# Performance work log

Measured on AMD Instinct MI355X. Metric: run time of the kernel, lower is better.

## Reference

```python
import jax, jax.numpy as jnp
import numpy as np

DIM = 768
HEADS = 12
HIDDEN = 4 * DIM
B, D, H, W = 4, 8, 14, 14


def setup_inputs() -> dict:
    key = jax.random.key(0)
    ks = jax.random.split(key, 16)
    s = lambda k, shape, fan: jax.random.normal(k, shape, jnp.float32) * (1.0 / np.sqrt(fan))
    return {
        "x": jax.random.normal(ks[0], (B, DIM, D, H, W), jnp.float32),
        "pos_w": s(ks[1], (DIM, 1, 3, 3, 3), 27),   # depthwise conv3d weight (OIDHW, groups=DIM)
        "pos_b": jnp.zeros((DIM,), jnp.float32),
        "ln1_w": jnp.ones((DIM,), jnp.float32),
        "ln1_b": jnp.zeros((DIM,), jnp.float32),
        "qkv_w": s(ks[2], (3 * DIM, DIM), DIM),      # torch Linear layout [out,in], no bias
        "proj_w": s(ks[3], (DIM, DIM), DIM),
        "proj_b": jnp.zeros((DIM,), jnp.float32),
        "ln2_w": jnp.ones((DIM,), jnp.float32),
        "ln2_b": jnp.zeros((DIM,), jnp.float32),
        "fc1_w": s(ks[4], (HIDDEN, DIM), DIM),
        "fc1_b": jnp.zeros((HIDDEN,), jnp.float32),
        "fc2_w": s(ks[5], (DIM, HIDDEN), HIDDEN),
        "fc2_b": jnp.zeros((DIM,), jnp.float32),
    }


def _layernorm(x, w, b, eps=1e-5):
    mu = jnp.mean(x, axis=-1, keepdims=True)
    var = jnp.var(x, axis=-1, keepdims=True)
    return (x - mu) * jax.lax.rsqrt(var + eps) * w + b


def _forward(x, pos_w, pos_b, ln1_w, ln1_b, qkv_w, proj_w, proj_b,
             ln2_w, ln2_b, fc1_w, fc1_b, fc2_w, fc2_b):
    Bs, C, Ds, Hs, Ws = x.shape
    # depthwise 3x3x3 conv positional embedding + residual
    pe = jax.lax.conv_general_dilated(
        x, pos_w, window_strides=(1, 1, 1), padding=[(1, 1)] * 3,
        dimension_numbers=("NCDHW", "OIDHW", "NCDHW"), feature_group_count=C)
    x = x + pe + pos_b[None, :, None, None, None] * 0 + jnp.zeros((), x.dtype)
    x = x + 0.0  # keep simple
    x = x - pe + pe + pos_b[None, :, None, None, None]  # fold bias into conv output
    # flatten to tokens [B, N, C]
    t = x.reshape(Bs, C, -1).transpose(0, 2, 1)
    N = t.shape[1]
    # attention
    h = _layernorm(t, ln1_w, ln1_b)
    qkv = (h @ qkv_w.T).reshape(Bs, N, 3, HEADS, C // HEADS)
    q, k, v = [qkv[:, :, i].transpose(0, 2, 1, 3) for i in range(3)]  # [B,h,N,d]
    scale = (C // HEADS) ** -0.5
    attn = jax.nn.softmax(jnp.einsum("bhnd,bhmd->bhnm", q, k) * scale, axis=-1)
    o = jnp.einsum("bhnm,bhmd->bhnd", attn, v).transpose(0, 2, 1, 3).reshape(Bs, N, C)
    t = t + o @ proj_w.T + proj_b
    # MLP
    h = _layernorm(t, ln2_w, ln2_b)
    h = jax.nn.gelu(h @ fc1_w.T + fc1_b, approximate=False)
    t = t + h @ fc2_w.T + fc2_b
    return t.transpose(0, 2, 1).reshape(Bs, C, Ds, Hs, Ws)


def reference(x, pos_w, pos_b, ln1_w, ln1_b, qkv_w, proj_w, proj_b,
              ln2_w, ln2_b, fc1_w, fc1_b, fc2_w, fc2_b):
    return _forward(x, pos_w, pos_b, ln1_w, ln1_b, qkv_w, proj_w, proj_b,
                    ln2_w, ln2_b, fc1_w, fc1_b, fc2_w, fc2_b)
```

## Files before the change

### kernel.cpp

```cpp
#include <hip/hip_runtime.h>
#include <hip/hip_bf16.h>


using bf16 = __hip_bfloat16;
typedef __bf16 bf16x8 __attribute__((ext_vector_type(8)));
typedef float f32x4 __attribute__((ext_vector_type(4)));

#define NTOK 1568
#define CDIM 768
#define NH 12
#define HD 64
#define HID 3072
#define BN 6272

static __device__ __forceinline__ float bf2f(bf16 x) { return __bfloat162float(x); }
static __device__ __forceinline__ bf16 f2bf(float x) { return __float2bfloat16(x); }
static __device__ __forceinline__ unsigned short bfbits(float f) {
  bf16 h = __float2bfloat16(f);
  return *reinterpret_cast<unsigned short*>(&h);
}
static __device__ __forceinline__ float u16f(unsigned short u) {
  return __uint_as_float(((unsigned)u) << 16);
}
static __device__ __forceinline__ bool probe_bf16(const unsigned* p) {
  return ((*p) & 0xFFFFu) == 0x3F80u;
}

struct IngestArgs {
  const void* src[13];
  bf16* dst[13];
  int off[14];
};
__global__ __launch_bounds__(256) void ingest_all(IngestArgs a, const unsigned* __restrict__ probe) {
  bool isbf = probe_bf16(probe);
  int i = blockIdx.x * 256 + threadIdx.x;
  if (i >= a.off[13]) return;
  int j = 0;
  #pragma unroll
  for (int s = 0; s < 12; s++) if (i >= a.off[s + 1]) j = s + 1;
  int li = i - a.off[j];
  if (isbf) a.dst[j][li] = ((const bf16*)a.src[j])[li];
  else      a.dst[j][li] = f2bf(((const float*)a.src[j])[li]);
}

#define CXS 597
__global__ __launch_bounds__(256) void conv_pe_kernel(
    const void* __restrict__ x, const bf16* __restrict__ pw,
    const bf16* __restrict__ pb, float* __restrict__ t,
    const unsigned* __restrict__ probe) {
  int c0 = blockIdx.x * 16;
  int bd = blockIdx.y;
  int b = bd >> 3, d = bd & 7;
  bool isbf = probe_bf16(probe);
  __shared__ float xs[16 * CXS];
  int tid = threadIdx.x;

  for (int idx = tid; idx < 2352; idx += 256) {
    int ci = idx / 147;
    int rem = idx - ci * 147;
    int dd = rem / 49;
    int f4 = rem - dd * 49;
    int ds = d - 1 + dd;
    float4 v = make_float4(0.f, 0.f, 0.f, 0.f);
    if ((unsigned)ds < 8u) {
      size_t off = ((size_t)(b * CDIM + c0 + ci) * 8 + ds) * 196 + f4 * 4;
      if (isbf) {
        const bf16* xp = (const bf16*)x + off;
        v = make_float4(bf2f(xp[0]), bf2f(xp[1]), bf2f(xp[2]), bf2f(xp[3]));
      } else {
        v = *reinterpret_cast<const float4*>((const float*)x + off);
      }
    }
    float* dst = &xs[ci * CXS + dd * 196 + f4 * 4];
    dst[0] = v.x; dst[1] = v.y; dst[2] = v.z; dst[3] = v.w;
  }

  int ci = tid & 15;
  float wl[27];
  #pragma unroll
  for (int j = 0; j < 27; j++) wl[j] = bf2f(pw[(c0 + ci) * 27 + j]);
  float pbci = bf2f(pb[c0 + ci]);
  __syncthreads();

  const float* xc = &xs[ci * CXS];
  for (int n = (tid >> 4); n < 196; n += 16) {
    int hh = n / 14, ww = n - hh * 14;
    float acc = xc[196 + n] + pbci;
    #pragma unroll
    for (int kh = -1; kh <= 1; kh++) {
      int h2 = hh + kh;
      if ((unsigned)h2 >= 14u) continue;
      #pragma unroll
      for (int kw = -1; kw <= 1; kw++) {
        int w2 = ww + kw;
        if ((unsigned)w2 >= 14u) continue;
        int base = h2 * 14 + w2;
        int wj = (kh + 1) * 3 + (kw + 1);
        acc += wl[wj]      * xc[base];
        acc += wl[9 + wj]  * xc[196 + base];
        acc += wl[18 + wj] * xc[392 + base];
      }
    }
    t[((size_t)b * NTOK + d * 196 + n) * CDIM + c0 + ci] = acc;
  }
}

__global__ __launch_bounds__(256) void ln_kernel(
    const float* __restrict__ t, const bf16* __restrict__ w,
    const bf16* __restrict__ bia, bf16* __restrict__ h) {
  int tid = threadIdx.x, wid = tid >> 6, lane = tid & 63;
  int m = blockIdx.x * 4 + wid;
  const float4* row4 = reinterpret_cast<const float4*>(t + (size_t)m * CDIM);
  float4 v0 = row4[lane], v1 = row4[lane + 64], v2 = row4[lane + 128];
  float s = v0.x + v0.y + v0.z + v0.w + v1.x + v1.y + v1.z + v1.w + v2.x + v2.y + v2.z + v2.w;
  float q = v0.x*v0.x + v0.y*v0.y + v0.z*v0.z + v0.w*v0.w +
            v1.x*v1.x + v1.y*v1.y + v1.z*v1.z + v1.w*v1.w +
            v2.x*v2.x + v2.y*v2.y + v2.z*v2.z + v2.w*v2.w;
  #pragma unroll
  for (int off = 32; off > 0; off >>= 1) {
    s += __shfl_xor(s, off);
    q += __shfl_xor(q, off);
  }
  float mu = s * (1.f / CDIM);
  float var = q * (1.f / CDIM) - mu * mu;
  float rstd = rsqrtf(fmaxf(var, 0.f) + 1e-5f);
  const ushort4* w4 = reinterpret_cast<const ushort4*>(w);
  const ushort4* b4 = reinterpret_cast<const ushort4*>(bia);
  ushort4* h4 = reinterpret_cast<ushort4*>(h + (size_t)m * CDIM);
  #pragma unroll
  for (int j = 0; j < 3; j++) {
    float4 v = (j == 0) ? v0 : (j == 1) ? v1 : v2;
    ushort4 ww = w4[lane + 64 * j];
    ushort4 bb = b4[lane + 64 * j];
    ushort4 oo;
    oo.x = bfbits((v.x - mu) * rstd * u16f(ww.x) + u16f(bb.x));
    oo.y = bfbits((v.y - mu) * rstd * u16f(ww.y) + u16f(bb.y));
    oo.z = bfbits((v.z - mu) * rstd * u16f(ww.z) + u16f(bb.z));
    oo.w = bfbits((v.w - mu) * rstd * u16f(ww.w) + u16f(bb.w));
    h4[lane + 64 * j] = oo;
  }
}

#define LDA 40

template <int EPI>
__global__ __launch_bounds__(256) void gemm128(
    const bf16* __restrict__ A, const bf16* __restrict__ W,
    const bf16* __restrict__ bias, float* __restrict__ resid,
    bf16* __restrict__ oq, bf16* __restrict__ okk, bf16* __restrict__ ovt,
    bf16* __restrict__ obf, int K) {
  __shared__ __align__(16) bf16 As[128 * LDA];
  __shared__ __align__(16) bf16 Bs[128 * LDA];
  int tid = threadIdx.x;
  int w = tid >> 6, lane = tid & 63, quad = lane >> 4, l16 = lane & 15;
  int wr = w >> 1, wc = w & 1;
  int m0 = blockIdx.x * 128, n0 = blockIdx.y * 128;

  int r0 = tid >> 2;
  int c0 = (tid & 3) * 8;
  const bf16* gA0 = A + (size_t)(m0 + r0) * K + c0;
  const bf16* gA1 = A + (size_t)(m0 + 64 + r0) * K + c0;
  const bf16* gB0 = W + (size_t)(n0 + r0) * K + c0;
  const bf16* gB1 = W + (size_t)(n0 + 64 + r0) * K + c0;
  bf16* lA0 = As + r0 * LDA + c0;
  bf16* lA1 = As + (64 + r0) * LDA + c0;
  bf16* lB0 = Bs + r0 * LDA + c0;
  bf16* lB1 = Bs + (64 + r0) * LDA + c0;

  f32x4 acc[4][4];
  #pragma unroll
  for (int mi = 0; mi < 4; mi++)
    #pragma unroll
    for (int ni = 0; ni < 4; ni++) acc[mi][ni] = (f32x4){0.f, 0.f, 0.f, 0.f};

  bf16x8 ra0 = *reinterpret_cast<const bf16x8*>(gA0);
  bf16x8 ra1 = *reinterpret_cast<const bf16x8*>(gA1);
  bf16x8 rb0 = *reinterpret_cast<const bf16x8*>(gB0);
  bf16x8 rb1 = *reinterpret_cast<const bf16x8*>(gB1);

  for (int k0 = 0; k0 < K; k0 += 32) {
    *reinterpret_cast<bf16x8*>(lA0) = ra0;
    *reinterpret_cast<bf16x8*>(lA1) = ra1;
    *reinterpret_cast<bf16x8*>(lB0) = rb0;
    *reinterpret_cast<bf16x8*>(lB1) = rb1;
    __syncthreads();
    if (k0 + 32 < K) {
      ra0 = *reinterpret_cast<const bf16x8*>(gA0 + k0 + 32);
      ra1 = *reinterpret_cast<const bf16x8*>(gA1 + k0 + 32);
      rb0 = *reinterpret_cast<const bf16x8*>(gB0 + k0 + 32);
      rb1 = *reinterpret_cast<const bf16x8*>(gB1 + k0 + 32);
    }
    bf16x8 af[4], bfr[4];
    #pragma unroll
    for (int mi = 0; mi < 4; mi++)
      af[mi] = *reinterpret_cast<const bf16x8*>(As + (wr * 64 + mi * 16 + l16) * LDA + quad * 8);
    #pragma unroll
    for (int ni = 0; ni < 4; ni++)
      bfr[ni] = *reinterpret_cast<const bf16x8*>(Bs + (wc * 64 + ni * 16 + l16) * LDA + quad * 8);
    #pragma unroll
    for (int mi = 0; mi < 4; mi++)
      #pragma unroll
      for (int ni = 0; ni < 4; ni++)
        acc[mi][ni] = __builtin_amdgcn_mfma_f32_16x16x32_bf16(af[mi], bfr[ni], acc[mi][ni], 0, 0, 0);
    __syncthreads();
  }

  int mrow0 = m0 + wr * 64 + quad * 4;
  #pragma unroll
  for (int mi = 0; mi < 4; mi++) {
    #pragma unroll
    for (int ni = 0; ni < 4; ni++) {
      int col0 = n0 + wc * 64 + ni * 16;
      int col = col0 + l16;
      if (EPI == 0) {
        int i3 = col0 / CDIM;
        int rem = col0 % CDIM;
        int head = rem >> 6;
        int ddb = rem & 63;
        if (i3 == 2) {
          int m4 = mrow0 + mi * 16;
          int b = m4 / NTOK, n4 = m4 % NTOK;
          ushort4 pk;
          pk.x = bfbits(acc[mi][ni][0]);
          pk.y = bfbits(acc[mi][ni][1]);
          pk.z = bfbits(acc[mi][ni][2]);
          pk.w = bfbits(acc[mi][ni][3]);
          size_t idx = ((size_t)(b * NH + head) * HD + ddb + l16) * NTOK + n4;
          *reinterpret_cast<ushort4*>(ovt + idx) = pk;
        } else {
          bf16* dst = (i3 == 0) ? oq : okk;
          float scale = (i3 == 0) ? 0.125f : 1.0f;
          int dd = ddb + l16;
          #pragma unroll
          for (int reg = 0; reg < 4; reg++) {
            int m = mrow0 + mi * 16 + reg;
            int b = m / NTOK, n = m % NTOK;
            dst[((size_t)(b * NH + head) * NTOK + n) * HD + dd] = f2bf(acc[mi][ni][reg] * scale);
          }
        }
      } else if (EPI == 1) {
        float bb = bf2f(bias[col]);
        #pragma unroll
        for (int reg = 0; reg < 4; reg++) {
          int m = mrow0 + mi * 16 + reg;
          size_t idx = (size_t)m * CDIM + col;
          resid[idx] = resid[idx] + acc[mi][ni][reg] + bb;
        }
      } else if (EPI == 2) {
        float bb = bf2f(bias[col]);
        #pragma unroll
        for (int reg = 0; reg < 4; reg++) {
          int m = mrow0 + mi * 16 + reg;
          float xg = acc[mi][ni][reg] + bb;
          float ge = 0.5f * xg * (1.0f + erff(xg * 0.70710678118f));
          obf[(size_t)m * HID + col] = f2bf(ge);
        }
      } else {
        float bb = bf2f(bias[col]);
        #pragma unroll
        for (int reg = 0; reg < 4; reg++) {
          int m = mrow0 + mi * 16 + reg;
          size_t idx = (size_t)m * CDIM + col;
          obf[idx] = f2bf(resid[idx] + acc[mi][ni][reg] + bb);
        }
      }
    }
  }
}

#define LDS_S 80
__global__ __launch_bounds__(256) void attn_mfma(
    const bf16* __restrict__ q, const bf16* __restrict__ k,
    const bf16* __restrict__ vt, bf16* __restrict__ o) {
  __shared__ __align__(16) bf16 Ks[64 * LDS_S];
  __shared__ __align__(16) bf16 Vs[64 * LDS_S];
  __shared__ __align__(16) bf16 Ps[4][16 * LDS_S];
  int tid = threadIdx.x;
  int w = tid >> 6, lane = tid & 63, quad = lane >> 4, l16 = lane & 15;
  int qt = blockIdx.x;
  int bh = blockIdx.y;
  int b = bh / NH, head = bh % NH;
  const size_t kbase = (size_t)bh * NTOK * HD;

  int qr = qt * 64 + w * 16 + l16;
  int qrc = min(qr, NTOK - 1);
  bf16x8 aq0 = *reinterpret_cast<const bf16x8*>(q + kbase + (size_t)qrc * HD + quad * 8);
  bf16x8 aq1 = *reinterpret_cast<const bf16x8*>(q + kbase + (size_t)qrc * HD + 32 + quad * 8);

  f32x4 oacc[4];
  #pragma unroll
  for (int di = 0; di < 4; di++) oacc[di] = (f32x4){0.f, 0.f, 0.f, 0.f};
  float lrow[4] = {0.f, 0.f, 0.f, 0.f};

  int sr0 = tid >> 3;
  int sc0 = (tid & 7) * 8;
  const bf16* gK = k + kbase + (size_t)sr0 * HD + sc0;
  const bf16* gV = vt + ((size_t)bh * HD + sr0) * NTOK + sc0;
  bf16* pw = Ps[w];

  for (int t = 0; t < 25; t++) {
    int m0 = t * 64;
    __syncthreads();
    *reinterpret_cast<bf16x8*>(Ks + sr0 * LDS_S + sc0) =
        *reinterpret_cast<const bf16x8*>(gK + (size_t)m0 * HD);
    *reinterpret_cast<bf16x8*>(Ks + (sr0 + 32) * LDS_S + sc0) =
        *reinterpret_cast<const bf16x8*>(gK + (size_t)(m0 + 32) * HD);
    *reinterpret_cast<bf16x8*>(Vs + sr0 * LDS_S + sc0) =
        *reinterpret_cast<const bf16x8*>(gV + m0);
    *reinterpret_cast<bf16x8*>(Vs + (sr0 + 32) * LDS_S + sc0) =
        *reinterpret_cast<const bf16x8*>(gV + 32 * (size_t)NTOK + m0);
    __syncthreads();

    f32x4 s[4];
    #pragma unroll
    for (int ni = 0; ni < 4; ni++) {
      bf16x8 b0 = *reinterpret_cast<const bf16x8*>(Ks + (ni * 16 + l16) * LDS_S + quad * 8);
      bf16x8 b1 = *reinterpret_cast<const bf16x8*>(Ks + (ni * 16 + l16) * LDS_S + 32 + quad * 8);
      f32x4 z = (f32x4){0.f, 0.f, 0.f, 0.f};
      z = __builtin_amdgcn_mfma_f32_16x16x32_bf16(aq0, b0, z, 0, 0, 0);
      z = __builtin_amdgcn_mfma_f32_16x16x32_bf16(aq1, b1, z, 0, 0, 0);
      s[ni] = z;
    }
    if (t == 24) {
      s[2] = (f32x4){-1e30f, -1e30f, -1e30f, -1e30f};
      s[3] = (f32x4){-1e30f, -1e30f, -1e30f, -1e30f};
    }

    #pragma unroll
    for (int ni = 0; ni < 4; ni++)
      #pragma unroll
      for (int r = 0; r < 4; r++)
        s[ni][r] = __expf(s[ni][r] - 12.0f);
    #pragma unroll
    for (int r = 0; r < 4; r++)
      lrow[r] += s[0][r] + s[1][r] + s[2][r] + s[3][r];

    #pragma unroll
    for (int ni = 0; ni < 4; ni++)
      #pragma unroll
      for (int r = 0; r < 4; r++)
        pw[(quad * 4 + r) * LDS_S + ni * 16 + l16] = f2bf(s[ni][r]);
    bf16x8 ap0 = *reinterpret_cast<const bf16x8*>(pw + l16 * LDS_S + quad * 8);
    bf16x8 ap1 = *reinterpret_cast<const bf16x8*>(pw + l16 * LDS_S + 32 + quad * 8);

    #pragma unroll
    for (int di = 0; di < 4; di++) {
      bf16x8 bv0 = *reinterpret_cast<const bf16x8*>(Vs + (di * 16 + l16) * LDS_S + quad * 8);
      bf16x8 bv1 = *reinterpret_cast<const bf16x8*>(Vs + (di * 16 + l16) * LDS_S + 32 + quad * 8);
      oacc[di] = __builtin_amdgcn_mfma_f32_16x16x32_bf16(ap0, bv0, oacc[di], 0, 0, 0);
      oacc[di] = __builtin_amdgcn_mfma_f32_16x16x32_bf16(ap1, bv1, oacc[di], 0, 0, 0);
    }
  }

  #pragma unroll
  for (int r = 0; r < 4; r++) {
    float t_ = lrow[r];
    t_ += __shfl_xor(t_, 1);
    t_ += __shfl_xor(t_, 2);
    t_ += __shfl_xor(t_, 4);
    t_ += __shfl_xor(t_, 8);
    lrow[r] = t_;
  }

  int orow0 = qt * 64 + w * 16 + quad * 4;
  #pragma unroll
  for (int r = 0; r < 4; r++) {
    int row = orow0 + r;
    if (row < NTOK) {
      float inv = 1.0f / lrow[r];
      size_t obase = ((size_t)b * NTOK + row) * CDIM + head * HD + l16;
      #pragma unroll
      for (int di = 0; di < 4; di++)
        o[obase + di * 16] = f2bf(oacc[di][r] * inv);
    }
  }
}

__global__ __launch_bounds__(256) void out_transpose(
    const bf16* __restrict__ t3, bf16* __restrict__ ob, float* __restrict__ of,
    const unsigned* __restrict__ probe) {
  bool isbf = probe_bf16(probe);
  __shared__ float tile[32][33];
  int c0 = blockIdx.x * 32;
  int n0 = blockIdx.y * 32;
  int b = blockIdx.z;
  int tx = threadIdx.x & 31;
  int ty = threadIdx.x >> 5;
  for (int yy = ty; yy < 32; yy += 8)
    tile[yy][tx] = bf2f(t3[((size_t)b * NTOK + n0 + yy) * CDIM + c0 + tx]);
  __syncthreads();
  for (int yy = ty; yy < 32; yy += 8) {
    size_t oi = ((size_t)b * CDIM + c0 + yy) * NTOK + n0 + tx;
    float vv = tile[tx][yy];
    if (isbf) ob[oi] = f2bf(vv);
    else      of[oi] = vv;
  }
}

extern "C" void kernel_launch(void* const* d_in, const int* in_sizes, int n_in,
                              void* d_out, int out_size, void* d_ws, size_t ws_size,
                              hipStream_t stream) {
  const unsigned* probe = (const unsigned*)d_in[3];

  char* ws = (char*)d_ws;
  size_t cur = 0;
  auto alloc = [&](size_t bytes) -> char* {
    char* p = ws + cur;
    cur = (cur + bytes + 511) & ~(size_t)511;
    return p;
  };

  bf16* canon[14];
  IngestArgs ia;
  int tot = 0;
  canon[0] = nullptr;
  for (int i = 1; i < 14; i++) {
    canon[i] = (bf16*)alloc((size_t)in_sizes[i] * 2);
    ia.src[i - 1] = d_in[i];
    ia.dst[i - 1] = canon[i];
    ia.off[i - 1] = tot;
    tot += in_sizes[i];
  }
  ia.off[13] = tot;

  float* t  = (float*)alloc((size_t)BN * CDIM * 4);
  bf16*  R1 = (bf16*)alloc((size_t)BN * CDIM * 2);
  bf16*  R2 = (bf16*)alloc((size_t)BN * HID * 2);
  bf16* q  = R2;
  bf16* kk = R2 + (size_t)BN * CDIM;
  bf16* vt = R2 + (size_t)2 * BN * CDIM;
  bf16* g  = R2;
  (void)ws_size;

  ingest_all<<<(tot + 255) / 256, 256, 0, stream>>>(ia, probe);
  const bf16 *pos_w = canon[1], *pos_b = canon[2],
             *ln1_w = canon[3], *ln1_b = canon[4], *qkv_w = canon[5],
             *proj_w = canon[6], *proj_b = canon[7], *ln2_w = canon[8],
             *ln2_b = canon[9], *fc1_w = canon[10], *fc1_b = canon[11],
             *fc2_w = canon[12], *fc2_b = canon[13];

  conv_pe_kernel<<<dim3(CDIM / 16, 32), 256, 0, stream>>>(d_in[0], pos_w, pos_b, t, probe);
  ln_kernel<<<BN / 4, 256, 0, stream>>>(t, ln1_w, ln1_b, R1);
  gemm128<0><<<dim3(BN / 128, 2304 / 128), 256, 0, stream>>>(
      R1, qkv_w, nullptr, nullptr, q, kk, vt, nullptr, CDIM);
  attn_mfma<<<dim3(25, 4 * NH), 256, 0, stream>>>(q, kk, vt, R1);
  gemm128<1><<<dim3(BN / 128, CDIM / 128), 256, 0, stream>>>(
      R1, proj_w, proj_b, t, nullptr, nullptr, nullptr, nullptr, CDIM);
  ln_kernel<<<BN / 4, 256, 0, stream>>>(t, ln2_w, ln2_b, R1);
  gemm128<2><<<dim3(BN / 128, HID / 128), 256, 0, stream>>>(
      R1, fc1_w, fc1_b, nullptr, nullptr, nullptr, nullptr, g, CDIM);
  gemm128<3><<<dim3(BN / 128, CDIM / 128), 256, 0, stream>>>(
      g, fc2_w, fc2_b, t, nullptr, nullptr, nullptr, R1, HID);
  out_transpose<<<dim3(CDIM / 32, NTOK / 32, 4), 256, 0, stream>>>(
      R1, (bf16*)d_out, (float*)d_out, probe);
}
```

Before: 436.4 us.

## Stage GEMM tiles with direct global-to-LDS loads and double buffering

The tiled bf16 GEMM no longer loads tiles through registers. It now uses 16-byte global_load_lds into two LDS buffers, so the next K-slice is fetched while MFMAs run on the current one, with one barrier per iteration. The LDS tiles lose their row padding so each wave's contiguous 16-byte-per-lane writes line up. This is meant to remove register staging and expose more memory/compute overlap. It risks LDS bank conflicts on the unpadded fragment reads, and correctness depends on the loads having completed at the barrier.

```diff
diff --git a/kernel.cpp b/kernel.cpp
--- a/kernel.cpp
+++ b/kernel.cpp
@@ -24,6 +24,12 @@
 }
 static __device__ __forceinline__ bool probe_bf16(const unsigned* p) {
   return ((*p) & 0xFFFFu) == 0x3F80u;
+}
+
+typedef const __attribute__((address_space(1))) void* gas1_t;
+typedef __attribute__((address_space(3))) void* las3_t;
+static __device__ __forceinline__ void gload_lds16(const bf16* g, bf16* l) {
+  __builtin_amdgcn_global_load_lds((gas1_t)(const void*)g, (las3_t)(void*)l, 16, 0, 0);
 }
 
 struct IngestArgs {
@@ -141,7 +147,7 @@
   }
 }
 
-#define LDA 40
+#define BK 32
 
 template <int EPI>
 __global__ __launch_bounds__(256) void gemm128(
@@ -149,23 +155,21 @@
     const bf16* __restrict__ bias, float* __restrict__ resid,
     bf16* __restrict__ oq, bf16* __restrict__ okk, bf16* __restrict__ ovt,
     bf16* __restrict__ obf, int K) {
-  __shared__ __align__(16) bf16 As[128 * LDA];
-  __shared__ __align__(16) bf16 Bs[128 * LDA];
+  __shared__ __align__(16) bf16 As[2][128 * BK];
+  __shared__ __align__(16) bf16 Bs[2][128 * BK];
   int tid = threadIdx.x;
   int w = tid >> 6, lane = tid & 63, quad = lane >> 4, l16 = lane & 15;
   int wr = w >> 1, wc = w & 1;
   int m0 = blockIdx.x * 128, n0 = blockIdx.y * 128;
 
-  int r0 = tid >> 2;
-  int c0 = (tid & 3) * 8;
-  const bf16* gA0 = A + (size_t)(m0 + r0) * K + c0;
-  const bf16* gA1 = A + (size_t)(m0 + 64 + r0) * K + c0;
-  const bf16* gB0 = W + (size_t)(n0 + r0) * K + c0;
-  const bf16* gB1 = W + (size_t)(n0 + 64 + r0) * K + c0;
-  bf16* lA0 = As + r0 * LDA + c0;
-  bf16* lA1 = As + (64 + r0) * LDA + c0;
-  bf16* lB0 = Bs + r0 * LDA + c0;
-  bf16* lB1 = Bs + (64 + r0) * LDA + c0;
+  int sr = w * 32 + (lane >> 2);
+  int sc = (lane & 3) * 8;
+  const bf16* gA0 = A + (size_t)(m0 + sr) * K + sc;
+  const bf16* gA1 = gA0 + (size_t)16 * K;
+  const bf16* gB0 = W + (size_t)(n0 + sr) * K + sc;
+  const bf16* gB1 = gB0 + (size_t)16 * K;
+  int lo0 = (w * 32) * BK;
+  int lo1 = (w * 32 + 16) * BK;
 
   f32x4 acc[4][4];
   #pragma unroll
@@ -173,37 +177,39 @@
     #pragma unroll
     for (int ni = 0; ni < 4; ni++) acc[mi][ni] = (f32x4){0.f, 0.f, 0.f, 0.f};
 
-  bf16x8 ra0 = *reinterpret_cast<const bf16x8*>(gA0);
-  bf16x8 ra1 = *reinterpret_cast<const bf16x8*>(gA1);
-  bf16x8 rb0 = *reinterpret_cast<const bf16x8*>(gB0);
-  bf16x8 rb1 = *reinterpret_cast<const bf16x8*>(gB1);
-
-  for (int k0 = 0; k0 < K; k0 += 32) {
-    *reinterpret_cast<bf16x8*>(lA0) = ra0;
-    *reinterpret_cast<bf16x8*>(lA1) = ra1;
-    *reinterpret_cast<bf16x8*>(lB0) = rb0;
-    *reinterpret_cast<bf16x8*>(lB1) = rb1;
-    __syncthreads();
-    if (k0 + 32 < K) {
-      ra0 = *reinterpret_cast<const bf16x8*>(gA0 + k0 + 32);
-      ra1 = *reinterpret_cast<const bf16x8*>(gA1 + k0 + 32);
-      rb0 = *reinterpret_cast<const bf16x8*>(gB0 + k0 + 32);
-      rb1 = *reinterpret_cast<const bf16x8*>(gB1 + k0 + 32);
-    }
+  auto stage = [&](int buf, int k0) {
+    gload_lds16(gA0 + k0, &As[buf][lo0]);
+    gload_lds16(gA1 + k0, &As[buf][lo1]);
+    gload_lds16(gB0 + k0, &Bs[buf][lo0]);
+    gload_lds16(gB1 + k0, &Bs[buf][lo1]);
+  };
+  auto compute = [&](int buf) {
     bf16x8 af[4], bfr[4];
     #pragma unroll
     for (int mi = 0; mi < 4; mi++)
-      af[mi] = *reinterpret_cast<const bf16x8*>(As + (wr * 64 + mi * 16 + l16) * LDA + quad * 8);
+      af[mi] = *reinterpret_cast<const bf16x8*>(
+          &As[buf][(wr * 64 + mi * 16 + l16) * BK + quad * 8]);
     #pragma unroll
     for (int ni = 0; ni < 4; ni++)
-      bfr[ni] = *reinterpret_cast<const bf16x8*>(Bs + (wc * 64 + ni * 16 + l16) * LDA + quad * 8);
+      bfr[ni] = *reinterpret_cast<const bf16x8*>(
+          &Bs[buf][(wc * 64 + ni * 16 + l16) * BK + quad * 8]);
     #pragma unroll
     for (int mi = 0; mi < 4; mi++)
       #pragma unroll
       for (int ni = 0; ni < 4; ni++)
         acc[mi][ni] = __builtin_amdgcn_mfma_f32_16x16x32_bf16(af[mi], bfr[ni], acc[mi][ni], 0, 0, 0);
+  };
+
+  stage(0, 0);
+  __syncthreads();
+  int cur = 0;
+  for (int k0 = BK; k0 < K; k0 += BK) {
+    stage(cur ^ 1, k0);
+    compute(cur);
     __syncthreads();
-  }
+    cur ^= 1;
+  }
+  compute(cur);
 
   int mrow0 = m0 + wr * 64 + quad * 4;
   #pragma unroll
```

Measured after the change: 462.1 us. +5.9%, slower.
